# Performance work log

Hardware: AMD Instinct MI355X
Metric: run time of the kernel (lower is better)

Reference implementation:

```python
import jax, jax.numpy as jnp
import numpy as np

N_NODES = 50000
N_EDGES = 800000
D_IN = 128
HIDDEN = 64
N_CLASSES = 2


def gcn_conv(x, edge_index, W, b, num_nodes):
    """PyG GCNConv: linear (no bias) -> add self-loops -> sym-normalized aggregate -> + bias."""
    h = x @ W  # [N, H]
    loop = jnp.arange(num_nodes, dtype=edge_index.dtype)
    src = jnp.concatenate([edge_index[0], loop])  # [E+N]
    dst = jnp.concatenate([edge_index[1], loop])
    deg = jax.ops.segment_sum(jnp.ones_like(dst, dtype=h.dtype), dst, num_segments=num_nodes)
    dinv = jnp.where(deg > 0, jax.lax.rsqrt(deg), 0.0)
    norm = dinv[src] * dinv[dst]  # [E+N]
    msg = h[src] * norm[:, None]  # [E+N, H]  (gather + scale)
    out = jax.ops.segment_sum(msg, dst, num_segments=num_nodes)  # scatter-add
    return out + b


def setup_inputs() -> dict:
    key = jax.random.key(0)
    ks = jax.random.split(key, 6)
    x = jax.random.normal(ks[0], (N_NODES, D_IN), dtype=jnp.float32)
    edge_index = jax.random.randint(ks[1], (2, N_EDGES), 0, N_NODES, dtype=jnp.int64)
    # Glorot-ish init for weights, zero bias (PyG default)
    W1 = jax.random.normal(ks[2], (D_IN, HIDDEN), dtype=jnp.float32) * (1.0 / np.sqrt(D_IN))
    b1 = jnp.zeros((HIDDEN,), dtype=jnp.float32)
    W2 = jax.random.normal(ks[3], (HIDDEN, N_CLASSES), dtype=jnp.float32) * (1.0 / np.sqrt(HIDDEN))
    b2 = jnp.zeros((N_CLASSES,), dtype=jnp.float32)
    return {"x": x, "edge_index": edge_index, "W1": W1, "b1": b1, "W2": W2, "b2": b2}


def reference(x, edge_index, W1, b1, W2, b2):
    h = jax.nn.relu(gcn_conv(x, edge_index, W1, b1, N_NODES))
    # F.dropout(training=self.training) is identity in eval mode
    out = gcn_conv(h, edge_index, W2, b2, N_NODES)
    return out
```

## Files before the change

kernel.cpp:

```cpp
#include <hip/hip_runtime.h>

#define N_NODES 50000
#define N_EDGES 800000
#define D_IN 128
#define HIDDEN 64
#define N_CLASSES 2
#define NBUK 782
#define NBUK_P 784
#define NBLK 196
#define NBLK_P 200
#define NE4 200000
#define XPAD 136

typedef _Float16 half4v __attribute__((ext_vector_type(4)));
typedef _Float16 h8 __attribute__((ext_vector_type(8)));
typedef float f4 __attribute__((ext_vector_type(4)));


__global__ __launch_bounds__(256) void k_hist(const int4* __restrict__ dst4,
                                              int* __restrict__ bhist) {
    __shared__ int hist[NBUK];
    int t = threadIdx.x;
    for (int i = t; i < NBUK; i += 256) hist[i] = 0;
    __syncthreads();
    int base4 = blockIdx.x * 1024;
#pragma unroll
    for (int k = 0; k < 4; k++) {
        int idx = base4 + k * 256 + t;
        if (idx < NE4) {
            int4 d = dst4[idx];
            atomicAdd(&hist[d.x >> 6], 1);
            atomicAdd(&hist[d.y >> 6], 1);
            atomicAdd(&hist[d.z >> 6], 1);
            atomicAdd(&hist[d.w >> 6], 1);
        }
    }
    __syncthreads();
    for (int i = t; i < NBUK; i += 256) bhist[blockIdx.x * NBUK_P + i] = hist[i];
}


__global__ __launch_bounds__(256) void k_colscan(const int* __restrict__ bhist,
                                                 int* __restrict__ excT,
                                                 int* __restrict__ colsum) {
    __shared__ int part[256];
    int b = blockIdx.x;
    int t = threadIdx.x;
    int v = (t < NBLK) ? bhist[t * NBUK_P + b] : 0;
    part[t] = v;
    __syncthreads();
    for (int off = 1; off < 256; off <<= 1) {
        int p = (t >= off) ? part[t - off] : 0;
        __syncthreads();
        part[t] += p;
        __syncthreads();
    }
    if (t < NBLK) excT[b * NBLK_P + t] = part[t] - v;
    if (t == 255) colsum[b] = part[255];
}


__global__ __launch_bounds__(256) void k_binA2s(const int4* __restrict__ src4,
                                                const int4* __restrict__ dst4,
                                                const int* __restrict__ excT,
                                                const int* __restrict__ colsum,
                                                int* __restrict__ bucket_off,
                                                int* __restrict__ row_ptr,
                                                int* __restrict__ ebin) {
    __shared__ int part[256];
    __shared__ int cur[NBUK];
    const int b = blockIdx.x;
    const int t = threadIdx.x;

    int v[4];
    int s = 0;
#pragma unroll
    for (int i = 0; i < 4; i++) {
        int idx = t * 4 + i;
        v[i] = (idx < NBUK) ? colsum[idx] : 0;
        s += v[i];
    }
    part[t] = s;
    __syncthreads();
    for (int off = 1; off < 256; off <<= 1) {
        int p = (t >= off) ? part[t - off] : 0;
        __syncthreads();
        part[t] += p;
        __syncthreads();
    }
    int run = (t == 0) ? 0 : part[t - 1];
#pragma unroll
    for (int i = 0; i < 4; i++) {
        int idx = t * 4 + i;
        if (idx < NBUK) {
            cur[idx] = run + excT[idx * NBLK_P + b];
            if (b == 0) bucket_off[idx] = run;
            run += v[i];
        } else if (idx == NBUK && b == 0) {
            bucket_off[idx] = run;
        }
    }
    if (b == 0 && t == 0) row_ptr[N_NODES] = N_EDGES;
    __syncthreads();

    int base4 = b * 1024;
#pragma unroll
    for (int k = 0; k < 4; k++) {
        int idx = base4 + k * 256 + t;
        if (idx < NE4) {
            int4 sv = src4[idx];
            int4 d = dst4[idx];
            int p0 = atomicAdd(&cur[d.x >> 6], 1);
            int p1 = atomicAdd(&cur[d.y >> 6], 1);
            int p2 = atomicAdd(&cur[d.z >> 6], 1);
            int p3 = atomicAdd(&cur[d.w >> 6], 1);
            ebin[p0] = (sv.x << 7) | (d.x & 63);
            ebin[p1] = (sv.y << 7) | (d.y & 63);
            ebin[p2] = (sv.z << 7) | (d.z & 63);
            ebin[p3] = (sv.w << 7) | (d.w & 63);
        }
    }
}


__global__ __launch_bounds__(256) void k_csr_gemm(
    const int* __restrict__ ebin, const int* __restrict__ bucket_off,
    const float* __restrict__ x, const float* __restrict__ W1,
    int* __restrict__ row_ptr, float* __restrict__ dinv_g,
    int* __restrict__ rec, _Float16* __restrict__ hs)
{
    __shared__ _Float16 xs[64 * XPAD];
    __shared__ _Float16 Wt[64 * XPAD];
    __shared__ int cnt[64];
    __shared__ int cur[64];
    __shared__ float sdinv[64];
    const int b = blockIdx.x;
    const int t = threadIdx.x;
    const int row0 = b * 64;

    for (int i4 = t; i4 < 64 * D_IN / 4; i4 += 256) {
        int r = i4 >> 5;
        int k4 = (i4 & 31) << 2;
        int grow = row0 + r;
        half4v hv;
        if (grow < N_NODES) {
            float4 v = *(const float4*)&x[grow * D_IN + k4];
            hv.x = (_Float16)v.x; hv.y = (_Float16)v.y;
            hv.z = (_Float16)v.z; hv.w = (_Float16)v.w;
        } else {
            hv.x = hv.y = hv.z = hv.w = (_Float16)0.f;
        }
        *(half4v*)&xs[r * XPAD + k4] = hv;
    }
    for (int i4 = t; i4 < D_IN * HIDDEN / 4; i4 += 256) {
        float4 v = *(const float4*)&W1[i4 * 4];
        int k = i4 >> 4;
        int n = (i4 & 15) << 2;
        Wt[(n + 0) * XPAD + k] = (_Float16)v.x;
        Wt[(n + 1) * XPAD + k] = (_Float16)v.y;
        Wt[(n + 2) * XPAD + k] = (_Float16)v.z;
        Wt[(n + 3) * XPAD + k] = (_Float16)v.w;
    }

    if (t < 64) cnt[t] = 0;
    __syncthreads();
    int beg = bucket_off[b], end = bucket_off[b + 1];
    for (int i = beg + t; i < end; i += 256) atomicAdd(&cnt[ebin[i] & 63], 1);
    __syncthreads();
    if (t < 64) {
        int deg = cnt[t];
        int sum = deg;
#pragma unroll
        for (int off = 1; off < 64; off <<= 1) {
            int v = __shfl_up(sum, off, 64);
            if (t >= off) sum += v;
        }
        int rp = beg + sum - deg;
        cur[t] = rp;
        float di = rsqrtf((float)(deg + 1));
        sdinv[t] = di;
        int node = row0 + t;
        if (node < N_NODES) {
            row_ptr[node] = rp;
            dinv_g[node] = di;
        }
    }
    __syncthreads();
    for (int i = beg + t; i < end; i += 256) {
        int pk = ebin[i];
        int pos = atomicAdd(&cur[pk & 63], 1);
        rec[pos] = pk >> 7;
    }
    __syncthreads();

    const int w = t >> 6;
    const int L = t & 63;
    const int mrow = w * 16 + (L & 15);
    const int qk = (L >> 4) * 8;
    f4 acc0 = {0.f, 0.f, 0.f, 0.f}, acc1 = acc0, acc2 = acc0, acc3 = acc0;
#pragma unroll
    for (int ks = 0; ks < D_IN; ks += 32) {
        h8 a = *(const h8*)&xs[mrow * XPAD + ks + qk];
        h8 b0 = *(const h8*)&Wt[(0 * 16 + (L & 15)) * XPAD + ks + qk];
        h8 b1 = *(const h8*)&Wt[(1 * 16 + (L & 15)) * XPAD + ks + qk];
        h8 b2 = *(const h8*)&Wt[(2 * 16 + (L & 15)) * XPAD + ks + qk];
        h8 b3 = *(const h8*)&Wt[(3 * 16 + (L & 15)) * XPAD + ks + qk];
        acc0 = __builtin_amdgcn_mfma_f32_16x16x32_f16(a, b0, acc0, 0, 0, 0);
        acc1 = __builtin_amdgcn_mfma_f32_16x16x32_f16(a, b1, acc1, 0, 0, 0);
        acc2 = __builtin_amdgcn_mfma_f32_16x16x32_f16(a, b2, acc2, 0, 0, 0);
        acc3 = __builtin_amdgcn_mfma_f32_16x16x32_f16(a, b3, acc3, 0, 0, 0);
    }

    const int n0 = L & 15;
#pragma unroll
    for (int j = 0; j < 4; j++) {
        int m = w * 16 + (L >> 4) * 4 + j;
        float di = sdinv[m];
        size_t base = (size_t)(row0 + m) * HIDDEN;
        hs[base + 0 * 16 + n0] = (_Float16)(acc0[j] * di);
        hs[base + 1 * 16 + n0] = (_Float16)(acc1[j] * di);
        hs[base + 2 * 16 + n0] = (_Float16)(acc2[j] * di);
        hs[base + 3 * 16 + n0] = (_Float16)(acc3[j] * di);
    }
}


__global__ __launch_bounds__(256) void k_agg1_l2(
    const _Float16* __restrict__ hs, const int* __restrict__ row_ptr,
    const int* __restrict__ rec, const float* __restrict__ dinv,
    const float* __restrict__ b1, const float* __restrict__ W2,
    float* __restrict__ zs)
{
    const int node = blockIdx.x * 4 + (threadIdx.x >> 6);
    const int lane = threadIdx.x & 63;
    const int q = lane >> 4;
    const int f = lane & 15;
    const half4v* H = (const half4v*)hs;

    float di = dinv[node];
    float4 acc = make_float4(0.f, 0.f, 0.f, 0.f);

    int beg = row_ptr[node];
    int end = row_ptr[node + 1];

    for (int base = beg; base < end; base += 64) {
        int n = end - base;
        if (n > 64) n = 64;
        int r = N_NODES;
        if (lane < n) r = rec[base + lane];
        int n16 = (n + 15) & ~15;
        for (int e = 0; e < n16; e += 16) {
            int s0 = __shfl(r, e + q, 64);
            int s1 = __shfl(r, e + 4 + q, 64);
            int s2 = __shfl(r, e + 8 + q, 64);
            int s3 = __shfl(r, e + 12 + q, 64);
            half4v a0 = H[s0 * 16 + f];
            half4v a1 = H[s1 * 16 + f];
            half4v a2 = H[s2 * 16 + f];
            half4v a3 = H[s3 * 16 + f];
            acc.x += (float)a0.x + (float)a1.x + (float)a2.x + (float)a3.x;
            acc.y += (float)a0.y + (float)a1.y + (float)a2.y + (float)a3.y;
            acc.z += (float)a0.z + (float)a1.z + (float)a2.z + (float)a3.z;
            acc.w += (float)a0.w + (float)a1.w + (float)a2.w + (float)a3.w;
        }
    }

    acc.x += __shfl_xor(acc.x, 16, 64);
    acc.y += __shfl_xor(acc.y, 16, 64);
    acc.z += __shfl_xor(acc.z, 16, 64);
    acc.w += __shfl_xor(acc.w, 16, 64);
    acc.x += __shfl_xor(acc.x, 32, 64);
    acc.y += __shfl_xor(acc.y, 32, 64);
    acc.z += __shfl_xor(acc.z, 32, 64);
    acc.w += __shfl_xor(acc.w, 32, 64);

    half4v sv = H[node * 16 + f];
    acc.x += (float)sv.x;
    acc.y += (float)sv.y;
    acc.z += (float)sv.z;
    acc.w += (float)sv.w;

    float4 bb = ((const float4*)b1)[f];
    float4 y;
    y.x = fmaxf(fmaf(acc.x, di, bb.x), 0.f);
    y.y = fmaxf(fmaf(acc.y, di, bb.y), 0.f);
    y.z = fmaxf(fmaf(acc.z, di, bb.z), 0.f);
    y.w = fmaxf(fmaf(acc.w, di, bb.w), 0.f);
    float4 wA = ((const float4*)W2)[2 * f];
    float4 wB = ((const float4*)W2)[2 * f + 1];
    float p0 = y.x * wA.x + y.y * wA.z + y.z * wB.x + y.w * wB.z;
    float p1 = y.x * wA.y + y.y * wA.w + y.z * wB.y + y.w * wB.w;

    p0 += __shfl_down(p0, 8, 64);
    p1 += __shfl_down(p1, 8, 64);
    p0 += __shfl_down(p0, 4, 64);
    p1 += __shfl_down(p1, 4, 64);
    p0 += __shfl_down(p0, 2, 64);
    p1 += __shfl_down(p1, 2, 64);
    p0 += __shfl_down(p0, 1, 64);
    p1 += __shfl_down(p1, 1, 64);
    if (lane == 0) {
        zs[node * 2 + 0] = p0 * di;
        zs[node * 2 + 1] = p1 * di;
    }
}


__global__ __launch_bounds__(256) void k_agg2(
    const float* __restrict__ zs, const int* __restrict__ row_ptr,
    const int* __restrict__ rec, const float* __restrict__ dinv,
    const float* __restrict__ b2, float* __restrict__ out)
{
    int node = blockIdx.x * 4 + (threadIdx.x >> 6);
    int lane = threadIdx.x & 63;
    int beg = row_ptr[node];
    int end = row_ptr[node + 1];
    float a0 = 0.f, a1 = 0.f;
    for (int idx = beg + lane; idx < end; idx += 64) {
        int s = rec[idx];
        float2 v = *(const float2*)&zs[s * 2];
        a0 += v.x;
        a1 += v.y;
    }
#pragma unroll
    for (int off = 32; off > 0; off >>= 1) {
        a0 += __shfl_down(a0, off, 64);
        a1 += __shfl_down(a1, off, 64);
    }
    if (lane == 0) {
        float di = dinv[node];
        float2 zv = *(const float2*)&zs[node * 2];
        float2 o;
        o.x = fmaf(di, a0 + zv.x, b2[0]);
        o.y = fmaf(di, a1 + zv.y, b2[1]);
        *(float2*)&out[node * 2] = o;
    }
}


extern "C" void kernel_launch(void* const* d_in, const int* in_sizes, int n_in,
                              void* d_out, int out_size, void* d_ws, size_t ws_size,
                              hipStream_t stream) {
    const float* x  = (const float*)d_in[0];
    const int* ei   = (const int*)d_in[1];
    const float* W1 = (const float*)d_in[2];
    const float* b1 = (const float*)d_in[3];
    const float* W2 = (const float*)d_in[4];
    const float* b2 = (const float*)d_in[5];
    float* out = (float*)d_out;

    const int4* src4 = (const int4*)ei;
    const int4* dst4 = (const int4*)(ei + N_EDGES);

    int*      bucket_off = (int*)d_ws;
    int*      colsum     = (int*)d_ws + 1024;
    float*    dinv       = (float*)d_ws + 2048;
    int*      row_ptr    = (int*)d_ws + 52224;
    int*      bhist      = (int*)d_ws + 102432;
    int*      excT       = (int*)d_ws + 256128;
    int*      ebin       = (int*)d_ws + 412576;
    int*      rec        = (int*)d_ws + 1212576;
    _Float16* hs         = (_Float16*)((int*)d_ws + 2012576);
    float*    zs         = (float*)d_ws + 3614112;

    k_hist<<<NBLK, 256, 0, stream>>>(dst4, bhist);
    k_colscan<<<NBUK, 256, 0, stream>>>(bhist, excT, colsum);
    k_binA2s<<<NBLK, 256, 0, stream>>>(src4, dst4, excT, colsum, bucket_off, row_ptr, ebin);
    k_csr_gemm<<<NBUK, 256, 0, stream>>>(ebin, bucket_off, x, W1, row_ptr, dinv, rec, hs);
    k_agg1_l2<<<N_NODES / 4, 256, 0, stream>>>(hs, row_ptr, rec, dinv, b1, W2, zs);
    k_agg2<<<N_NODES / 4, 256, 0, stream>>>(zs, row_ptr, rec, dinv, b2, out);
}
```

Measured before the change: 139.7 us.

## Map fewer lanes per node in both aggregation kernels

Measured after the change: 132.0 us. -5.5%, faster.

```diff
diff --git a/kernel.cpp b/kernel.cpp
--- a/kernel.cpp
+++ b/kernel.cpp
@@ -231,10 +231,11 @@
     const float* __restrict__ b1, const float* __restrict__ W2,
     float* __restrict__ zs)
 {
-    const int node = blockIdx.x * 4 + (threadIdx.x >> 6);
-    const int lane = threadIdx.x & 63;
-    const int q = lane >> 4;
-    const int f = lane & 15;
+    const int node = blockIdx.x * 8 + (threadIdx.x >> 5);
+    const int hl = threadIdx.x & 31;
+    const int q = hl >> 4;
+    const int f = hl & 15;
+    const int hbase = threadIdx.x & 32;
     const half4v* H = (const half4v*)hs;
 
     float di = dinv[node];
@@ -243,25 +244,38 @@
     int beg = row_ptr[node];
     int end = row_ptr[node + 1];
 
-    for (int base = beg; base < end; base += 64) {
+    for (int base = beg; base < end; base += 32) {
         int n = end - base;
-        if (n > 64) n = 64;
+        if (n > 32) n = 32;
         int r = N_NODES;
-        if (lane < n) r = rec[base + lane];
+        if (hl < n) r = rec[base + hl];
         int n16 = (n + 15) & ~15;
         for (int e = 0; e < n16; e += 16) {
-            int s0 = __shfl(r, e + q, 64);
-            int s1 = __shfl(r, e + 4 + q, 64);
-            int s2 = __shfl(r, e + 8 + q, 64);
-            int s3 = __shfl(r, e + 12 + q, 64);
+            int i0 = hbase + e + q;
+            int s0 = __shfl(r, i0 + 0, 64);
+            int s1 = __shfl(r, i0 + 2, 64);
+            int s2 = __shfl(r, i0 + 4, 64);
+            int s3 = __shfl(r, i0 + 6, 64);
+            int s4 = __shfl(r, i0 + 8, 64);
+            int s5 = __shfl(r, i0 + 10, 64);
+            int s6 = __shfl(r, i0 + 12, 64);
+            int s7 = __shfl(r, i0 + 14, 64);
             half4v a0 = H[s0 * 16 + f];
             half4v a1 = H[s1 * 16 + f];
             half4v a2 = H[s2 * 16 + f];
             half4v a3 = H[s3 * 16 + f];
-            acc.x += (float)a0.x + (float)a1.x + (float)a2.x + (float)a3.x;
-            acc.y += (float)a0.y + (float)a1.y + (float)a2.y + (float)a3.y;
-            acc.z += (float)a0.z + (float)a1.z + (float)a2.z + (float)a3.z;
-            acc.w += (float)a0.w + (float)a1.w + (float)a2.w + (float)a3.w;
+            half4v a4 = H[s4 * 16 + f];
+            half4v a5 = H[s5 * 16 + f];
+            half4v a6 = H[s6 * 16 + f];
+            half4v a7 = H[s7 * 16 + f];
+            acc.x += ((float)a0.x + (float)a1.x) + ((float)a2.x + (float)a3.x)
+                   + ((float)a4.x + (float)a5.x) + ((float)a6.x + (float)a7.x);
+            acc.y += ((float)a0.y + (float)a1.y) + ((float)a2.y + (float)a3.y)
+                   + ((float)a4.y + (float)a5.y) + ((float)a6.y + (float)a7.y);
+            acc.z += ((float)a0.z + (float)a1.z) + ((float)a2.z + (float)a3.z)
+                   + ((float)a4.z + (float)a5.z) + ((float)a6.z + (float)a7.z);
+            acc.w += ((float)a0.w + (float)a1.w) + ((float)a2.w + (float)a3.w)
+                   + ((float)a4.w + (float)a5.w) + ((float)a6.w + (float)a7.w);
         }
     }
 
@@ -269,10 +283,6 @@
     acc.y += __shfl_xor(acc.y, 16, 64);
     acc.z += __shfl_xor(acc.z, 16, 64);
     acc.w += __shfl_xor(acc.w, 16, 64);
-    acc.x += __shfl_xor(acc.x, 32, 64);
-    acc.y += __shfl_xor(acc.y, 32, 64);
-    acc.z += __shfl_xor(acc.z, 32, 64);
-    acc.w += __shfl_xor(acc.w, 32, 64);
 
     half4v sv = H[node * 16 + f];
     acc.x += (float)sv.x;
@@ -299,7 +309,7 @@
     p1 += __shfl_down(p1, 2, 64);
     p0 += __shfl_down(p0, 1, 64);
     p1 += __shfl_down(p1, 1, 64);
-    if (lane == 0) {
+    if (hl == 0) {
         zs[node * 2 + 0] = p0 * di;
         zs[node * 2 + 1] = p1 * di;
     }
@@ -311,23 +321,26 @@
     const int* __restrict__ rec, const float* __restrict__ dinv,
     const float* __restrict__ b2, float* __restrict__ out)
 {
-    int node = blockIdx.x * 4 + (threadIdx.x >> 6);
-    int lane = threadIdx.x & 63;
+    const int node = blockIdx.x * 16 + (threadIdx.x >> 4);
+    const int j = threadIdx.x & 15;
     int beg = row_ptr[node];
     int end = row_ptr[node + 1];
     float a0 = 0.f, a1 = 0.f;
-    for (int idx = beg + lane; idx < end; idx += 64) {
+    for (int idx = beg + j; idx < end; idx += 16) {
         int s = rec[idx];
         float2 v = *(const float2*)&zs[s * 2];
         a0 += v.x;
         a1 += v.y;
     }
-#pragma unroll
-    for (int off = 32; off > 0; off >>= 1) {
-        a0 += __shfl_down(a0, off, 64);
-        a1 += __shfl_down(a1, off, 64);
-    }
-    if (lane == 0) {
+    a0 += __shfl_down(a0, 8, 64);
+    a1 += __shfl_down(a1, 8, 64);
+    a0 += __shfl_down(a0, 4, 64);
+    a1 += __shfl_down(a1, 4, 64);
+    a0 += __shfl_down(a0, 2, 64);
+    a1 += __shfl_down(a1, 2, 64);
+    a0 += __shfl_down(a0, 1, 64);
+    a1 += __shfl_down(a1, 1, 64);
+    if (j == 0) {
         float di = dinv[node];
         float2 zv = *(const float2*)&zs[node * 2];
         float2 o;
@@ -367,6 +380,6 @@
     k_colscan<<<NBUK, 256, 0, stream>>>(bhist, excT, colsum);
     k_binA2s<<<NBLK, 256, 0, stream>>>(src4, dst4, excT, colsum, bucket_off, row_ptr, ebin);
     k_csr_gemm<<<NBUK, 256, 0, stream>>>(ebin, bucket_off, x, W1, row_ptr, dinv, rec, hs);
-    k_agg1_l2<<<N_NODES / 4, 256, 0, stream>>>(hs, row_ptr, rec, dinv, b1, W2, zs);
-    k_agg2<<<N_NODES / 4, 256, 0, stream>>>(zs, row_ptr, rec, dinv, b2, out);
-}
+    k_agg1_l2<<<N_NODES / 8, 256, 0, stream>>>(hs, row_ptr, rec, dinv, b1, W2, zs);
+    k_agg2<<<N_NODES / 16, 256, 0, stream>>>(zs, row_ptr, rec, dinv, b2, out);
+}
```
